# Optimization experiments

Hardware: AMD Instinct MI355X
Metric: run time of the kernel (lower is better)

The kernel has to match this reference:

```python
import jax, jax.numpy as jnp
import numpy as np
from jax import lax

T, B = 80, 32
ACT, CIN, HID, LSTM_H = 16, 4, 512, 256

def _conv(x, w, b, stride, pad):
    y = lax.conv_general_dilated(x, w, (stride, stride), [(pad, pad), (pad, pad)],
                                 dimension_numbers=('NCHW', 'OIHW', 'NCHW'))
    return y + b[None, :, None, None]

def setup_inputs() -> dict:
    key = jax.random.key(0)
    ks = jax.random.split(key, 20)
    s = 0.02
    return {
        'x': jax.random.uniform(ks[0], (T, B, CIN, 84, 84), dtype=jnp.float32),
        'last_action': jax.random.randint(ks[1], (T, B), 0, ACT),
        'reward': jax.random.normal(ks[2], (T, B), dtype=jnp.float32),
        'dones': jnp.zeros((T, B), dtype=bool),
        'hx': jax.random.normal(ks[3], (2, B, LSTM_H), dtype=jnp.float32) * s,
        'conv1_w': jax.random.normal(ks[4], (32, CIN, 8, 8), jnp.float32) * s,
        'conv1_b': jnp.zeros((32,), jnp.float32),
        'conv2_w': jax.random.normal(ks[5], (64, 32, 4, 4), jnp.float32) * s,
        'conv2_b': jnp.zeros((64,), jnp.float32),
        'conv3_w': jax.random.normal(ks[6], (64, 64, 3, 3), jnp.float32) * s,
        'conv3_b': jnp.zeros((64,), jnp.float32),
        'fc_w': jax.random.normal(ks[7], (HID, 3136), jnp.float32) * s,
        'fc_b': jnp.zeros((HID,), jnp.float32),
        'lstm_wih': jax.random.normal(ks[8], (4 * LSTM_H, HID + ACT + 1), jnp.float32) * s,
        'lstm_whh': jax.random.normal(ks[9], (4 * LSTM_H, LSTM_H), jnp.float32) * s,
        'lstm_bih': jnp.zeros((4 * LSTM_H,), jnp.float32),
        'lstm_bhh': jnp.zeros((4 * LSTM_H,), jnp.float32),
        'actor_w': jax.random.normal(ks[10], (ACT, LSTM_H), jnp.float32) * s,
        'actor_b': jnp.zeros((ACT,), jnp.float32),
        'critic_w': jax.random.normal(ks[11], (1, LSTM_H), jnp.float32) * s,
        'critic_b': jnp.zeros((1,), jnp.float32),
    }

def reference(x, last_action, reward, dones, hx,
              conv1_w, conv1_b, conv2_w, conv2_b, conv3_w, conv3_b,
              fc_w, fc_b, lstm_wih, lstm_whh, lstm_bih, lstm_bhh,
              actor_w, actor_b, critic_w, critic_b):
    seq_len, bs = x.shape[0], x.shape[1]
    xf = x.reshape(seq_len * bs, CIN, 84, 84)          # combine time & batch
    la = jax.nn.one_hot(last_action.reshape(-1), ACT, dtype=jnp.float32)
    rw = reward.reshape(-1, 1)

    lrelu = lambda v: jax.nn.leaky_relu(v, 0.01)
    h = lrelu(_conv(xf, conv1_w, conv1_b, 4, 1))       # [N,32,20,20]
    h = lrelu(_conv(h, conv2_w, conv2_b, 2, 0))        # [N,64,9,9]
    h = lrelu(_conv(h, conv3_w, conv3_b, 1, 0))        # [N,64,7,7]
    h = h.reshape(h.shape[0], -1)                      # [N,3136]
    h = lrelu(h @ fc_w.T + fc_b)                       # [N,512]
    h = jnp.concatenate([h, rw, la], axis=1)           # [N,529]
    h = h.reshape(seq_len, bs, -1)

    def step(carry, inp):
        xt, dt = inp                                   # [bs,529], [bs] bool
        carry = jnp.where(dt[None, :, None], 0.0, carry)
        hh, cc = carry[0], carry[1]
        gates = xt @ lstm_wih.T + lstm_bih + hh @ lstm_whh.T + lstm_bhh
        i, f, g, o = jnp.split(gates, 4, axis=1)
        cc = jax.nn.sigmoid(f) * cc + jax.nn.sigmoid(i) * jnp.tanh(g)
        hh = jax.nn.sigmoid(o) * jnp.tanh(cc)
        return jnp.stack([hh, cc], 0), hh

    _, hs = lax.scan(step, hx, (h, dones))             # hs: [T,bs,256]
    feat = hs.reshape(seq_len * bs, LSTM_H)

    logits = feat @ actor_w.T + actor_b                # [N,16]
    values = feat @ critic_w.T + critic_b              # [N,1]
    logits = jnp.where(jnp.isnan(logits), jnp.float32(1e-12), logits)
    return logits.reshape(seq_len, -1, bs), values.reshape(seq_len, bs)
```

## Files before the change

kernel.cpp:

```cpp
#include <hip/hip_runtime.h>
#include <math.h>

#define T_ 80
#define B_ 32
#define N_ 2560
#define LH_ 256

typedef __attribute__((ext_vector_type(8))) short short8;
typedef __attribute__((ext_vector_type(4))) float f32x4;
#define MFMA16(a, b, c) __builtin_amdgcn_mfma_f32_16x16x32_bf16((a), (b), (c), 0, 0, 0)

__device__ __forceinline__ float lrelu(float v) { return v > 0.f ? v : 0.01f * v; }
__device__ __forceinline__ short f2bf(float f) {
    unsigned u = __float_as_uint(f);
    return (short)((u + 0x7fffu + ((u >> 16) & 1u)) >> 16);
}

__global__ void pack_all_k(const float* __restrict__ c1w, const float* __restrict__ c2w,
                           const float* __restrict__ c3w, const float* __restrict__ fcw,
                           const float* __restrict__ wih,
                           short* __restrict__ wp1, short* __restrict__ wp2,
                           short* __restrict__ wp3, short* __restrict__ wfcP,
                           short* __restrict__ wihP, int* __restrict__ cnt) {
    int blk = blockIdx.x, tidx = threadIdx.x;
    if (blk < 6272) {
        int g = blk * 256 + tidx;
        int j = g / 3136, kp = g % 3136, p = kp >> 6, oc = kp & 63;
        wfcP[g] = f2bf(fcw[j * 3136 + oc * 49 + p]);
        return;
    }
    blk -= 6272;
    if (blk < 2048) {
        int g = blk * 256 + tidx;
        int r = g >> 9, k = g & 511;
        wihP[g] = f2bf(wih[r * 529 + k]);
        return;
    }
    blk -= 2048;
    if (blk < 32) {
        int g = blk * 256 + tidx;
        int ky = g >> 10, oc = (g >> 5) & 31, k = g & 31, kx = k >> 2, ci = k & 3;
        wp1[g] = f2bf(c1w[((oc * 4 + ci) * 8 + ky) * 8 + kx]);
        return;
    }
    blk -= 32;
    if (blk < 128) {
        int g = blk * 256 + tidx;
        int t = g >> 11, oc = (g >> 5) & 63, ci = g & 31, ky = t >> 2, kx = t & 3;
        wp2[g] = f2bf(c2w[((oc * 32 + ci) * 4 + ky) * 4 + kx]);
        return;
    }
    blk -= 128;
    if (blk < 144) {
        int g = blk * 256 + tidx;
        int tkc = g >> 11, oc = (g >> 5) & 63, c32 = g & 31;
        int t = tkc >> 1, kc = tkc & 1, ky = t / 3, kx = t % 3;
        wp3[g] = f2bf(c3w[((oc * 64 + kc * 32 + c32) * 3 + ky) * 3 + kx]);
        return;
    }
    cnt[tidx] = 0; cnt[256 + tidx] = 0;
}

#define C1_RS 344
__global__ __launch_bounds__(512) void conv1_mfma(
    const float* __restrict__ x, const short* __restrict__ wp1,
    const float* __restrict__ bias, short* __restrict__ h1) {
    __shared__ short xs[44 * C1_RS];
    __shared__ short ob[208 * 32];
    int blk = blockIdx.x, n = blk >> 1, h = blk & 1, tid = threadIdx.x;
    for (int i = tid; i < 44 * 84; i += 512) {
        int ry = i / 84, xi4 = i % 84;
        int ci = xi4 / 21, x4 = xi4 % 21;
        int iy = ry + h * 40 - 1;
        if (iy < 0 || iy > 83) continue;
        float4 v = *(const float4*)(x + (size_t)(n * 4 + ci) * 7056 + iy * 84 + x4 * 4);
        int base = ry * C1_RS + (x4 * 4 + 1) * 4 + ci;
        xs[base] = f2bf(v.x); xs[base + 4] = f2bf(v.y);
        xs[base + 8] = f2bf(v.z); xs[base + 12] = f2bf(v.w);
    }
    for (int i = tid; i < 44 * 4; i += 512)
        xs[(i >> 2) * C1_RS + (i & 3)] = 0;
    if (h == 0) for (int i = tid; i < C1_RS; i += 512) xs[i] = 0;
    __syncthreads();

    int lane = tid & 63, wid = tid >> 6;
    int lr = lane & 15, kq = lane >> 4;
    short8 bfr[8][2];
#pragma unroll
    for (int ky = 0; ky < 8; ++ky)
#pragma unroll
        for (int nt = 0; nt < 2; ++nt)
            bfr[ky][nt] = *(const short8*)&wp1[((ky * 32) + nt * 16 + lr) * 32 + kq * 8];
    float b0 = bias[lr], b1 = bias[16 + lr];

    for (int t = wid; t < 13; t += 8) {
        int p = t * 16 + lr; if (p > 199) p = 199;
        int oy = p / 20, ox = p % 20;
        f32x4 acc0 = {0.f, 0.f, 0.f, 0.f}, acc1 = {0.f, 0.f, 0.f, 0.f};
#pragma unroll
        for (int ky = 0; ky < 8; ++ky) {
            int ry = oy * 4 + ky;
            short8 af = *(const short8*)&xs[ry * C1_RS + ox * 16 + kq * 8];
            acc0 = MFMA16(af, bfr[ky][0], acc0);
            acc1 = MFMA16(af, bfr[ky][1], acc1);
        }
        int pm = t * 16 + kq * 4;
#pragma unroll
        for (int r = 0; r < 4; ++r) {
            ob[(pm + r) * 32 + lr]      = f2bf(lrelu(acc0[r] + b0));
            ob[(pm + r) * 32 + 16 + lr] = f2bf(lrelu(acc1[r] + b1));
        }
    }
    __syncthreads();
    uint4* dst = (uint4*)(h1 + (size_t)n * 12800 + h * 6400);
    for (int i = tid; i < 800; i += 512) dst[i] = ((uint4*)ob)[i];
}

__global__ __launch_bounds__(512) void conv23_mfma(
    const short* __restrict__ h1,
    const short* __restrict__ wp2, const float* __restrict__ b2v,
    const short* __restrict__ wp3, const float* __restrict__ b3v,
    short* __restrict__ h3) {
    __shared__ short in_s[400 * 40];
    __shared__ short ob2[96 * 72];
    int n = blockIdx.x, tid = threadIdx.x;
    const uint4* src = (const uint4*)(h1 + (size_t)n * 12800);
    for (int i = tid; i < 1600; i += 512)
        *(uint4*)&in_s[(i >> 2) * 40 + (i & 3) * 8] = src[i];
    __syncthreads();
    int lane = tid & 63, wid = tid >> 6;
    int nt = wid & 3, mh = wid >> 2;
    int lr = lane & 15, kq = lane >> 4;
    {
        short8 bfr[16];
#pragma unroll
        for (int t = 0; t < 16; ++t)
            bfr[t] = *(const short8*)&wp2[(t * 64 + nt * 16 + lr) * 32 + kq * 8];
        float bl = b2v[nt * 16 + lr];
        for (int mt = mh * 3; mt < mh * 3 + 3; ++mt) {
            int p = mt * 16 + lr; if (p > 80) p = 80;
            int oy = p / 9, ox = p % 9;
            f32x4 acc = {0.f, 0.f, 0.f, 0.f};
#pragma unroll
            for (int ky = 0; ky < 4; ++ky)
#pragma unroll
                for (int kx = 0; kx < 4; ++kx) {
                    int pix = (oy * 2 + ky) * 20 + ox * 2 + kx;
                    short8 af = *(const short8*)&in_s[pix * 40 + kq * 8];
                    acc = MFMA16(af, bfr[ky * 4 + kx], acc);
                }
            int pm = mt * 16 + kq * 4;
#pragma unroll
            for (int r = 0; r < 4; ++r)
                ob2[(pm + r) * 72 + nt * 16 + lr] = f2bf(lrelu(acc[r] + bl));
        }
    }
    __syncthreads();
    {
        short8 cfr[18];
#pragma unroll
        for (int t = 0; t < 18; ++t)
            cfr[t] = *(const short8*)&wp3[(t * 64 + nt * 16 + lr) * 32 + kq * 8];
        float bl3 = b3v[nt * 16 + lr];
        short* ob3 = in_s;
        for (int mt = mh * 2; mt < mh * 2 + 2; ++mt) {
            int p = mt * 16 + lr; if (p > 48) p = 48;
            int oy = p / 7, ox = p % 7;
            f32x4 acc = {0.f, 0.f, 0.f, 0.f};
#pragma unroll
            for (int ky = 0; ky < 3; ++ky)
#pragma unroll
                for (int kx = 0; kx < 3; ++kx) {
                    int pix = (oy + ky) * 9 + ox + kx;
#pragma unroll
                    for (int kc = 0; kc < 2; ++kc) {
                        short8 af = *(const short8*)&ob2[pix * 72 + kc * 32 + kq * 8];
                        acc = MFMA16(af, cfr[(ky * 3 + kx) * 2 + kc], acc);
                    }
                }
            int pm = mt * 16 + kq * 4;
#pragma unroll
            for (int r = 0; r < 4; ++r)
                ob3[(pm + r) * 64 + nt * 16 + lr] = f2bf(lrelu(acc[r] + bl3));
        }
    }
    __syncthreads();
    uint4* dst = (uint4*)(h3 + (size_t)n * 3136);
    for (int i = tid; i < 392; i += 512) dst[i] = ((uint4*)in_s)[i];
}

template <int OUT>
__global__ __launch_bounds__(256) void gemm_bf16(
    const short* __restrict__ A, const short* __restrict__ B,
    const float* __restrict__ bias, void* __restrict__ Cout,
    int M, int N, int K, int ldc,
    const float* __restrict__ reward = nullptr, const int* __restrict__ la = nullptr,
    const float* __restrict__ wih = nullptr, const float* __restrict__ bih = nullptr,
    const float* __restrict__ bhh = nullptr) {
    __shared__ short smem[15360];
    int m0 = blockIdx.y * 128, n0 = blockIdx.x * 64;
    int tid = threadIdx.x;
    int lane = tid & 63, wid = tid >> 6;
    int wr = wid >> 1, wc = wid & 1;
    int lr = lane & 15, kq = lane >> 4;
    f32x4 acc[4][2];
#pragma unroll
    for (int i = 0; i < 4; ++i)
#pragma unroll
        for (int j = 0; j < 2; ++j) acc[i][j] = (f32x4){0.f, 0.f, 0.f, 0.f};

    int nsteps = K >> 5;
#define STAGE(k0, buf)                                                          \
    {                                                                           \
        short* As = smem + (buf) * 5120;                                        \
        short* Bs = smem + 10240 + (buf) * 2560;                                \
        for (int i = tid; i < 512; i += 256) {                                  \
            int row = i >> 2, c4 = i & 3;                                       \
            *(uint4*)&As[row * 40 + c4 * 8] =                                   \
                *(const uint4*)&A[(size_t)(m0 + row) * K + (k0) + c4 * 8];      \
        }                                                                       \
        {                                                                       \
            int row = tid >> 2, c4 = tid & 3;                                   \
            *(uint4*)&Bs[row * 40 + c4 * 8] =                                   \
                *(const uint4*)&B[(size_t)(n0 + row) * K + (k0) + c4 * 8];      \
        }                                                                       \
    }
    STAGE(0, 0);
    __syncthreads();
    for (int ks = 0; ks < nsteps; ++ks) {
        int buf = ks & 1;
        if (ks + 1 < nsteps) STAGE((ks + 1) * 32, buf ^ 1);
        short* As = smem + buf * 5120;
        short* Bs = smem + 10240 + buf * 2560;
        short8 af[4], bfr[2];
#pragma unroll
        for (int i = 0; i < 4; ++i)
            af[i] = *(const short8*)&As[(wr * 64 + i * 16 + lr) * 40 + kq * 8];
#pragma unroll
        for (int j = 0; j < 2; ++j)
            bfr[j] = *(const short8*)&Bs[(wc * 32 + j * 16 + lr) * 40 + kq * 8];
#pragma unroll
        for (int i = 0; i < 4; ++i)
#pragma unroll
            for (int j = 0; j < 2; ++j)
                acc[i][j] = MFMA16(af[i], bfr[j], acc[i][j]);
        __syncthreads();
    }
#undef STAGE
    if (OUT == 2) {
        float* C = (float*)Cout;
#pragma unroll
        for (int i = 0; i < 4; ++i)
#pragma unroll
            for (int j = 0; j < 2; ++j) {
                int col = n0 + wc * 32 + j * 16 + lr;
                const float* wrow = wih + (size_t)col * 529;
                float base = bih[col] + bhh[col];
                float w512 = wrow[512];
#pragma unroll
                for (int r = 0; r < 4; ++r) {
                    int row = m0 + wr * 64 + i * 16 + kq * 4 + r;
                    C[(size_t)row * ldc + col] =
                        acc[i][j][r] + base + reward[row] * w512 + wrow[513 + la[row]];
                }
            }
    } else {
        short* ob = smem;
#pragma unroll
        for (int i = 0; i < 4; ++i)
#pragma unroll
            for (int j = 0; j < 2; ++j) {
                int col = wc * 32 + j * 16 + lr;
                float bl = bias[n0 + col];
#pragma unroll
                for (int r = 0; r < 4; ++r) {
                    int row = wr * 64 + i * 16 + kq * 4 + r;
                    ob[row * 64 + col] = f2bf(lrelu(acc[i][j][r] + bl));
                }
            }
        __syncthreads();
        short* C = (short*)Cout;
        for (int i = tid; i < 1024; i += 256) {
            int row = i >> 3, c8 = i & 7;
            *(uint4*)&C[(size_t)(m0 + row) * ldc + n0 + c8 * 8] =
                *(uint4*)&ob[row * 64 + c8 * 8];
        }
    }
}

__global__ __launch_bounds__(512) void lstm16_k(
    const float* __restrict__ gx,
    const float* __restrict__ whh,
    const unsigned char* __restrict__ dones,
    const float* __restrict__ hx,
    float* __restrict__ hs,
    unsigned short* __restrict__ hpub,
    int* __restrict__ cnt) {
    const int tid = threadIdx.x;
    const int grp  = blockIdx.x & 7;
    const int half = blockIdx.x >> 3;
    const int lane = tid & 63, w = tid >> 6;
    const int gt = w >> 1, s2 = w & 1;
    const int lr = lane & 15, kq = lane >> 4;

    __shared__ short hB[16 * 264];
    __shared__ float gate_s[4][128][4];

    short8 afr[4][8];
#pragma unroll
    for (int mi = 0; mi < 4; ++mi) {
        int row = gt * 256 + half * 128 + s2 * 64 + mi * 16 + lr;
        const float* wr = whh + (size_t)row * 256;
#pragma unroll
        for (int kt = 0; kt < 8; ++kt) {
            int k0 = kt * 32 + kq * 8;
            float4 a = *(const float4*)(wr + k0);
            float4 b = *(const float4*)(wr + k0 + 4);
            short8 f;
            f[0] = f2bf(a.x); f[1] = f2bf(a.y); f[2] = f2bf(a.z); f[3] = f2bf(a.w);
            f[4] = f2bf(b.x); f[5] = f2bf(b.y); f[6] = f2bf(b.z); f[7] = f2bf(b.w);
            afr[mi][kt] = f;
        }
    }
    {
        int* ap = (int*)afr;
#pragma unroll
        for (int i = 0; i < 128; ++i) asm volatile("" : "+v"(ap[i]));
    }

    for (int i = tid; i < 12 * 264; i += 512) hB[4 * 264 + i] = 0;

    const int u = tid >> 2, bt = tid & 3;
    const int b = grp * 4 + bt, gu = half * 128 + u;
    float cc = hx[(size_t)B_ * LH_ + b * LH_ + gu];

#pragma unroll
    for (int l = 0; l < 2; ++l) {
        int e = tid + l * 512;
        int bt2 = e >> 8, k = e & 255;
        int b2 = grp * 4 + bt2;
        float hv = hx[b2 * LH_ + k];
        if (dones[b2]) hv = 0.f;
        hB[bt2 * 264 + k] = f2bf(hv);
    }
    __syncthreads();

    const int mycnt = (grp * 2 + half) * 32, peercnt = (grp * 2 + (half ^ 1)) * 32;
    const int phalf = (half ^ 1) << 7;

    for (int t = 1; t <= T_; ++t) {
        const int nb0 = (t - 1) * B_;
        float gxv[4];
#pragma unroll
        for (int g2 = 0; g2 < 4; ++g2)
            gxv[g2] = gx[(size_t)(nb0 + b) * 1024 + g2 * 256 + gu];

        if (t > 1) {
            if (tid == 0) {
                while (__hip_atomic_load(&cnt[peercnt], __ATOMIC_ACQUIRE,
                                         __HIP_MEMORY_SCOPE_AGENT) < t - 1)
                    __builtin_amdgcn_s_sleep(1);
            }
            __syncthreads();
            int bt2 = tid >> 7, pu = tid & 127;
            int b2 = grp * 4 + bt2, pgu = phalf + pu;
            hB[bt2 * 264 + pgu] =
                (short)hpub[((t - 1) & 1) * 8192 + b2 * 256 + pgu];
        }
        __syncthreads();

        f32x4 acc[4] = {{0.f,0.f,0.f,0.f},{0.f,0.f,0.f,0.f},
                        {0.f,0.f,0.f,0.f},{0.f,0.f,0.f,0.f}};
#pragma unroll
        for (int kt = 0; kt < 8; ++kt) {
            short8 bfr = *(const short8*)&hB[lr * 264 + kt * 32 + kq * 8];
#pragma unroll
            for (int mi = 0; mi < 4; ++mi)
                acc[mi] = MFMA16(afr[mi][kt], bfr, acc[mi]);
        }
        if (lr < 4) {
#pragma unroll
            for (int mi = 0; mi < 4; ++mi)
#pragma unroll
                for (int r = 0; r < 4; ++r)
                    gate_s[gt][s2 * 64 + mi * 16 + kq * 4 + r][lr] = acc[mi][r];
        }
        __syncthreads();

        {
            bool dn = dones[nb0 + b] != 0;
            float gi = gate_s[0][u][bt] + gxv[0];
            float gf = gate_s[1][u][bt] + gxv[1];
            float gg = gate_s[2][u][bt] + gxv[2];
            float go = gate_s[3][u][bt] + gxv[3];
            float ccv = dn ? 0.f : cc;
            float si = 1.f / (1.f + expf(-gi));
            float sf = 1.f / (1.f + expf(-gf));
            float so = 1.f / (1.f + expf(-go));
            float c2 = sf * ccv + si * tanhf(gg);
            float h2 = so * tanhf(c2);
            cc = c2;
            hs[(size_t)(nb0 + b) * LH_ + gu] = h2;
            if (t < T_) {
                short hm = f2bf(dones[t * B_ + b] ? 0.f : h2);
                hB[bt * 264 + gu] = hm;
                hpub[(t & 1) * 8192 + b * 256 + gu] = (unsigned short)hm;
            }
        }
        __syncthreads();
        if (tid == 0)
            __hip_atomic_store(&cnt[mycnt], t, __ATOMIC_RELEASE,
                               __HIP_MEMORY_SCOPE_AGENT);
    }
}

__global__ void head_k(const float* __restrict__ hs,
                       const float* __restrict__ aw, const float* __restrict__ ab,
                       const float* __restrict__ cw, const float* __restrict__ cb,
                       float* __restrict__ out) {
    int gid = blockIdx.x * 256 + threadIdx.x;
    if (gid >= N_ * 17) return;
    int n = gid / 17, r = gid % 17;
    const float* f = hs + (size_t)n * 256;
    if (r < 16) {
        const float* w = aw + r * 256;
        float acc = ab[r];
        for (int k = 0; k < 256; ++k) acc = fmaf(f[k], w[k], acc);
        if (isnan(acc)) acc = 1e-12f;
        out[(size_t)n * 16 + r] = acc;
    } else {
        float acc = cb[0];
        for (int k = 0; k < 256; ++k) acc = fmaf(f[k], cw[k], acc);
        out[(size_t)N_ * 16 + n] = acc;
    }
}

extern "C" void kernel_launch(void* const* d_in, const int* in_sizes, int n_in,
                              void* d_out, int out_size, void* d_ws, size_t ws_size,
                              hipStream_t stream) {
    const float* x      = (const float*)d_in[0];
    const int* la       = (const int*)d_in[1];
    const float* reward = (const float*)d_in[2];
    const unsigned char* dones = (const unsigned char*)d_in[3];
    const float* hx     = (const float*)d_in[4];
    const float* c1w = (const float*)d_in[5];  const float* c1b = (const float*)d_in[6];
    const float* c2w = (const float*)d_in[7];  const float* c2b = (const float*)d_in[8];
    const float* c3w = (const float*)d_in[9];  const float* c3b = (const float*)d_in[10];
    const float* fcw = (const float*)d_in[11]; const float* fcb = (const float*)d_in[12];
    const float* wih = (const float*)d_in[13]; const float* whh = (const float*)d_in[14];
    const float* bih = (const float*)d_in[15]; const float* bhh = (const float*)d_in[16];
    const float* aw  = (const float*)d_in[17]; const float* ab  = (const float*)d_in[18];
    const float* cw  = (const float*)d_in[19]; const float* cb  = (const float*)d_in[20];

    char* wsb = (char*)d_ws;
    short* h1   = (short*)(wsb);
    short* h3   = (short*)(wsb + 92078080);
    short* hfc  = (short*)(wsb + 108134400);
    float* gx   = (float*)(wsb + 110755840);
    float* hs   = (float*)(wsb + 121241600);
    unsigned short* hpub = (unsigned short*)(wsb + 123863040);
    int*   cnt  = (int*)  (wsb + 123928576);
    short* wp1  = (short*)(wsb + 123932672);
    short* wp2  = (short*)(wsb + 123949056);
    short* wp3  = (short*)(wsb + 124014592);
    short* wfcP = (short*)(wsb + 124088320);
    short* wihP = (short*)(wsb + 127299584);

    pack_all_k<<<8625, 256, 0, stream>>>(c1w, c2w, c3w, fcw, wih,
                                         wp1, wp2, wp3, wfcP, wihP, cnt);

    conv1_mfma<<<5120, 512, 0, stream>>>(x, wp1, c1b, h1);
    conv23_mfma<<<2560, 512, 0, stream>>>(h1, wp2, c2b, wp3, c3b, h3);

    gemm_bf16<1><<<dim3(8, 20), 256, 0, stream>>>(h3, wfcP, fcb, hfc,
                                                  2560, 512, 3136, 512);
    gemm_bf16<2><<<dim3(16, 20), 256, 0, stream>>>(hfc, wihP, nullptr, gx,
                                                   2560, 1024, 512, 1024,
                                                   reward, la, wih, bih, bhh);

    lstm16_k<<<16, 512, 0, stream>>>(gx, whh, dones, hx, hs, hpub, cnt);
    head_k<<<170, 256, 0, stream>>>(hs, aw, ab, cw, cb, (float*)d_out);
}
```

Measured before the change: 528.6 us.

## Fuse conv1 into conv2/conv3 kernel, keeping conv1 output in shared memory

Merges the conv1 kernel into the conv2+conv3 kernel so each block computes conv1 for one image in two row passes, writing the activations straight into shared memory. This removes the global round trip of the h1 intermediate (about 65 MB of bf16 writes and reads) and one kernel launch. In exchange, grid parallelism halves (2560 blocks instead of 5120 for conv1), shared memory per block grows to roughly 75 KB, and the two conv1 passes run serially inside each block, which may reduce occupancy and latency hiding.

```diff
diff --git a/kernel.cpp b/kernel.cpp
--- a/kernel.cpp
+++ b/kernel.cpp
@@ -62,75 +62,72 @@
 }
 
 #define C1_RS 344
-__global__ __launch_bounds__(512) void conv1_mfma(
-    const float* __restrict__ x, const short* __restrict__ wp1,
-    const float* __restrict__ bias, short* __restrict__ h1) {
-    __shared__ short xs[44 * C1_RS];
-    __shared__ short ob[208 * 32];
-    int blk = blockIdx.x, n = blk >> 1, h = blk & 1, tid = threadIdx.x;
-    for (int i = tid; i < 44 * 84; i += 512) {
-        int ry = i / 84, xi4 = i % 84;
-        int ci = xi4 / 21, x4 = xi4 % 21;
-        int iy = ry + h * 40 - 1;
-        if (iy < 0 || iy > 83) continue;
-        float4 v = *(const float4*)(x + (size_t)(n * 4 + ci) * 7056 + iy * 84 + x4 * 4);
-        int base = ry * C1_RS + (x4 * 4 + 1) * 4 + ci;
-        xs[base] = f2bf(v.x); xs[base + 4] = f2bf(v.y);
-        xs[base + 8] = f2bf(v.z); xs[base + 12] = f2bf(v.w);
-    }
-    for (int i = tid; i < 44 * 4; i += 512)
-        xs[(i >> 2) * C1_RS + (i & 3)] = 0;
-    if (h == 0) for (int i = tid; i < C1_RS; i += 512) xs[i] = 0;
-    __syncthreads();
-
-    int lane = tid & 63, wid = tid >> 6;
-    int lr = lane & 15, kq = lane >> 4;
-    short8 bfr[8][2];
-#pragma unroll
-    for (int ky = 0; ky < 8; ++ky)
-#pragma unroll
-        for (int nt = 0; nt < 2; ++nt)
-            bfr[ky][nt] = *(const short8*)&wp1[((ky * 32) + nt * 16 + lr) * 32 + kq * 8];
-    float b0 = bias[lr], b1 = bias[16 + lr];
-
-    for (int t = wid; t < 13; t += 8) {
-        int p = t * 16 + lr; if (p > 199) p = 199;
-        int oy = p / 20, ox = p % 20;
-        f32x4 acc0 = {0.f, 0.f, 0.f, 0.f}, acc1 = {0.f, 0.f, 0.f, 0.f};
-#pragma unroll
-        for (int ky = 0; ky < 8; ++ky) {
-            int ry = oy * 4 + ky;
-            short8 af = *(const short8*)&xs[ry * C1_RS + ox * 16 + kq * 8];
-            acc0 = MFMA16(af, bfr[ky][0], acc0);
-            acc1 = MFMA16(af, bfr[ky][1], acc1);
-        }
-        int pm = t * 16 + kq * 4;
-#pragma unroll
-        for (int r = 0; r < 4; ++r) {
-            ob[(pm + r) * 32 + lr]      = f2bf(lrelu(acc0[r] + b0));
-            ob[(pm + r) * 32 + 16 + lr] = f2bf(lrelu(acc1[r] + b1));
-        }
-    }
-    __syncthreads();
-    uint4* dst = (uint4*)(h1 + (size_t)n * 12800 + h * 6400);
-    for (int i = tid; i < 800; i += 512) dst[i] = ((uint4*)ob)[i];
-}
-
-__global__ __launch_bounds__(512) void conv23_mfma(
-    const short* __restrict__ h1,
+__global__ __launch_bounds__(512) void conv123_mfma(
+    const float* __restrict__ x,
+    const short* __restrict__ wp1, const float* __restrict__ b1v,
     const short* __restrict__ wp2, const float* __restrict__ b2v,
     const short* __restrict__ wp3, const float* __restrict__ b3v,
     short* __restrict__ h3) {
-    __shared__ short in_s[400 * 40];
+    __shared__ short xs[44 * C1_RS];
+    __shared__ short h1s[400 * 40];
     __shared__ short ob2[96 * 72];
     int n = blockIdx.x, tid = threadIdx.x;
-    const uint4* src = (const uint4*)(h1 + (size_t)n * 12800);
-    for (int i = tid; i < 1600; i += 512)
-        *(uint4*)&in_s[(i >> 2) * 40 + (i & 3) * 8] = src[i];
-    __syncthreads();
     int lane = tid & 63, wid = tid >> 6;
+    int lr = lane & 15, kq = lane >> 4;
+
+    short8 bfr1[8][2];
+#pragma unroll
+    for (int ky = 0; ky < 8; ++ky)
+#pragma unroll
+        for (int nt = 0; nt < 2; ++nt)
+            bfr1[ky][nt] = *(const short8*)&wp1[((ky * 32) + nt * 16 + lr) * 32 + kq * 8];
+    float b0 = b1v[lr], b1 = b1v[16 + lr];
+
+#pragma unroll
+    for (int pass = 0; pass < 2; ++pass) {
+        const int iybase = pass ? 39 : -1;
+        for (int i = tid; i < 44 * 84; i += 512) {
+            int ry = i / 84, xi4 = i % 84;
+            int ci = xi4 / 21, x4 = xi4 % 21;
+            int iy = iybase + ry;
+            if (iy < 0) continue;
+            float4 v = *(const float4*)(x + (size_t)(n * 4 + ci) * 7056 + iy * 84 + x4 * 4);
+            int base = ry * C1_RS + (x4 * 4 + 1) * 4 + ci;
+            xs[base] = f2bf(v.x); xs[base + 4] = f2bf(v.y);
+            xs[base + 8] = f2bf(v.z); xs[base + 12] = f2bf(v.w);
+        }
+        for (int i = tid; i < 44 * 4; i += 512)
+            xs[(i >> 2) * C1_RS + (i & 3)] = 0;
+        if (pass == 0)
+            for (int i = tid; i < C1_RS; i += 512) xs[i] = 0;
+        __syncthreads();
+
+        for (int t = wid; t < 13; t += 8) {
+            int pl = t * 16 + lr; if (pl > 199) pl = 199;
+            int p = pass * 200 + pl;
+            int oy = p / 20, ox = p % 20;
+            f32x4 acc0 = {0.f, 0.f, 0.f, 0.f}, acc1 = {0.f, 0.f, 0.f, 0.f};
+#pragma unroll
+            for (int ky = 0; ky < 8; ++ky) {
+                int ry = oy * 4 + ky - (pass ? 40 : 0);
+                short8 af = *(const short8*)&xs[ry * C1_RS + ox * 16 + kq * 8];
+                acc0 = MFMA16(af, bfr1[ky][0], acc0);
+                acc1 = MFMA16(af, bfr1[ky][1], acc1);
+            }
+#pragma unroll
+            for (int r = 0; r < 4; ++r) {
+                int rp = t * 16 + kq * 4 + r;
+                if (rp < 200) {
+                    int row = pass * 200 + rp;
+                    h1s[row * 40 + lr]      = f2bf(lrelu(acc0[r] + b0));
+                    h1s[row * 40 + 16 + lr] = f2bf(lrelu(acc1[r] + b1));
+                }
+            }
+        }
+        __syncthreads();
+    }
+
     int nt = wid & 3, mh = wid >> 2;
-    int lr = lane & 15, kq = lane >> 4;
     {
         short8 bfr[16];
 #pragma unroll
@@ -146,7 +143,7 @@
 #pragma unroll
                 for (int kx = 0; kx < 4; ++kx) {
                     int pix = (oy * 2 + ky) * 20 + ox * 2 + kx;
-                    short8 af = *(const short8*)&in_s[pix * 40 + kq * 8];
+                    short8 af = *(const short8*)&h1s[pix * 40 + kq * 8];
                     acc = MFMA16(af, bfr[ky * 4 + kx], acc);
                 }
             int pm = mt * 16 + kq * 4;
@@ -162,7 +159,7 @@
         for (int t = 0; t < 18; ++t)
             cfr[t] = *(const short8*)&wp3[(t * 64 + nt * 16 + lr) * 32 + kq * 8];
         float bl3 = b3v[nt * 16 + lr];
-        short* ob3 = in_s;
+        short* ob3 = xs;
         for (int mt = mh * 2; mt < mh * 2 + 2; ++mt) {
             int p = mt * 16 + lr; if (p > 48) p = 48;
             int oy = p / 7, ox = p % 7;
@@ -186,7 +183,7 @@
     }
     __syncthreads();
     uint4* dst = (uint4*)(h3 + (size_t)n * 3136);
-    for (int i = tid; i < 392; i += 512) dst[i] = ((uint4*)in_s)[i];
+    for (int i = tid; i < 392; i += 512) dst[i] = ((uint4*)xs)[i];
 }
 
 template <int OUT>
@@ -453,7 +450,6 @@
     const float* cw  = (const float*)d_in[19]; const float* cb  = (const float*)d_in[20];
 
     char* wsb = (char*)d_ws;
-    short* h1   = (short*)(wsb);
     short* h3   = (short*)(wsb + 92078080);
     short* hfc  = (short*)(wsb + 108134400);
     float* gx   = (float*)(wsb + 110755840);
@@ -469,8 +465,7 @@
     pack_all_k<<<8625, 256, 0, stream>>>(c1w, c2w, c3w, fcw, wih,
                                          wp1, wp2, wp3, wfcP, wihP, cnt);
 
-    conv1_mfma<<<5120, 512, 0, stream>>>(x, wp1, c1b, h1);
-    conv23_mfma<<<2560, 512, 0, stream>>>(h1, wp2, c2b, wp3, c3b, h3);
+    conv123_mfma<<<2560, 512, 0, stream>>>(x, wp1, c1b, wp2, c2b, wp3, c3b, h3);
 
     gemm_bf16<1><<<dim3(8, 20), 256, 0, stream>>>(h3, wfcP, fcb, hfc,
                                                   2560, 512, 3136, 512);
```

After: 485.6 us. 1.09x faster.
